# Optimization experiments

Hardware: AMD Instinct MI355X
Metric: run time of the kernel (lower is better)

## Reference

```python
import jax, jax.numpy as jnp
import numpy as np

N, C_IN, C_OUT, T, V = 64, 64, 64, 300, 25


def setup_inputs() -> dict:
    key = jax.random.key(0)
    k1, k2, k3, k4 = jax.random.split(key, 4)
    x = jax.random.normal(k1, (N, C_IN, T, V), dtype=jnp.float32)
    a = jax.random.uniform(k2, (N, T, V, V), dtype=jnp.float32)
    # 1x1 Conv2D (channels_first) == per-pixel channel-mixing matmul
    W = jax.random.normal(k3, (C_IN, C_OUT), dtype=jnp.float32) * (1.0 / np.sqrt(C_IN))
    b = jax.random.normal(k4, (C_OUT,), dtype=jnp.float32) * 0.01
    return {"x": x, "a": a, "W": W, "b": b}


def reference(x, a, W, b):
    # 1x1 conv channels_first: mix channels at every (t, v) location
    y = jnp.einsum('nctv,cd->ndtv', x, W) + b[None, :, None, None]
    # dropout in eval mode (training=False) is identity
    # spatial graph convolution: node mixing with per-(n,t) adjacency
    out = jnp.einsum('nctv,ntvw->nctw', y, a)
    return (out, a)
```

## Files before the change

kernel.cpp:

```cpp
#include <hip/hip_runtime.h>


typedef __attribute__((ext_vector_type(8))) short short8;
typedef __attribute__((ext_vector_type(4))) float f32x4;

#define XS_S 66
#define YS_S 36
#define AT_S 36

__device__ __forceinline__ unsigned short f2bf(float f) {
    unsigned int u = __builtin_bit_cast(unsigned int, f);
    return (unsigned short)((u + 0x7FFFu + ((u >> 16) & 1u)) >> 16);
}

__global__ __launch_bounds__(512, 6)
void sgcn_fused(const float* __restrict__ xg, const float* __restrict__ ag,
                const float* __restrict__ Wg, const float* __restrict__ bg,
                float* __restrict__ outg)
{
    __shared__ alignas(16) unsigned short Wt[64 * XS_S];
    __shared__ alignas(16) unsigned short At[4 * 32 * AT_S];
    __shared__ alignas(16) unsigned short Ubuf[9216];

    const int tid  = threadIdx.x;
    const int wid  = tid >> 6;
    const int lane = tid & 63;
    const int q    = lane >> 4;
    const int lo   = lane & 15;

    const int bid = blockIdx.x;
    const int n   = bid / 75;
    const int t0  = (bid % 75) * 4;

    f32x4 xv[4];
    const long xbase = ((long)n * 64 * 300 + t0) * 25;
#pragma unroll
    for (int m = 0; m < 4; ++m) {
        const int f = tid + 512 * m;
        if (m < 3 || f < 1600) {
            const int c = f / 25, j = f % 25;
            xv[m] = *(const f32x4*)(xg + xbase + (long)c * 7500 + 4 * j);
        }
    }
    f32x4 av[2];
    const long abase = ((long)n * 300 + t0) * 625;
#pragma unroll
    for (int m = 0; m < 2; ++m) {
        const int f = tid + 512 * m;
        if (m < 1 || f < 625)
            av[m] = *(const f32x4*)(ag + abase + 4 * f);
    }
    f32x4 wv[2];
#pragma unroll
    for (int m = 0; m < 2; ++m)
        wv[m] = *(const f32x4*)(Wg + 4 * (tid + 512 * m));

    if (tid < 128) {
        unsigned short* ar = &At[(tid >> 5) * (32 * AT_S) + (tid & 31) * AT_S];
#pragma unroll
        for (int i = 25; i < 32; ++i) ar[i] = 0;
    }

#pragma unroll
    for (int m = 0; m < 2; ++m) {
        const int f = 4 * (tid + 512 * m);
#pragma unroll
        for (int i = 0; i < 4; ++i) {
            const int e = f + i, c = e >> 6, d = e & 63;
            Wt[d * XS_S + c] = f2bf(wv[m][i]);
        }
    }
#pragma unroll
    for (int m = 0; m < 4; ++m) {
        const int f = tid + 512 * m;
        if (m < 3 || f < 1600) {
            const int c = f / 25, j = f % 25;
#pragma unroll
            for (int i = 0; i < 4; ++i) {
                const int e = 4 * j + i;
                const int tl = e / 25, v = e % 25;
                Ubuf[tl * (32 * XS_S) + v * XS_S + c] = f2bf(xv[m][i]);
            }
        }
    }
    {
        float* aout = outg + 30720000L + abase;
#pragma unroll
        for (int m = 0; m < 2; ++m) {
            const int f = tid + 512 * m;
            if (m < 1 || f < 625) {
                *(f32x4*)(aout + 4 * f) = av[m];
#pragma unroll
                for (int i = 0; i < 4; ++i) {
                    const int e = 4 * f + i;
                    const int tl = e / 625, r = e % 625;
                    At[tl * (32 * AT_S) + (r % 25) * AT_S + (r / 25)] = f2bf(av[m][i]);
                }
            }
        }
    }
    __syncthreads();

    const int tl = wid >> 1;
    const int dh = wid & 1;
    const int t  = t0 + tl;
    const int d0 = 32 * dh;

    short8 wfrag[2][2];
#pragma unroll
    for (int mi = 0; mi < 2; ++mi)
#pragma unroll
        for (int ki = 0; ki < 2; ++ki)
            wfrag[mi][ki] = *(const short8*)&Wt[(d0 + 16 * mi + lo) * XS_S + 32 * ki + 8 * q];

    f32x4 bias[2];
#pragma unroll
    for (int mi = 0; mi < 2; ++mi)
#pragma unroll
        for (int r = 0; r < 4; ++r)
            bias[mi][r] = bg[d0 + 16 * mi + 4 * q + r];

    const unsigned short* xs = Ubuf + tl * (32 * XS_S);
    f32x4 accy[2][2];
#pragma unroll
    for (int mi = 0; mi < 2; ++mi) { accy[mi][0] = bias[mi]; accy[mi][1] = bias[mi]; }
#pragma unroll
    for (int ni = 0; ni < 2; ++ni)
#pragma unroll
        for (int ki = 0; ki < 2; ++ki) {
            const short8 bf = *(const short8*)&xs[(16 * ni + lo) * XS_S + 32 * ki + 8 * q];
#pragma unroll
            for (int mi = 0; mi < 2; ++mi)
                accy[mi][ni] = __builtin_amdgcn_mfma_f32_16x16x32_bf16(
                    wfrag[mi][ki], bf, accy[mi][ni], 0, 0, 0);
        }

    __syncthreads();

    unsigned short* ys = Ubuf + wid * (32 * YS_S);
#pragma unroll
    for (int mi = 0; mi < 2; ++mi)
#pragma unroll
        for (int ni = 0; ni < 2; ++ni) {
            const int v = 16 * ni + lo;
            const bool ok = (v < 25);
#pragma unroll
            for (int r = 0; r < 4; ++r)
                ys[(16 * mi + 4 * q + r) * YS_S + v] =
                    ok ? f2bf(accy[mi][ni][r]) : (unsigned short)0;
        }

    const unsigned short* at = At + tl * (32 * AT_S);
    short8 afr[2];
#pragma unroll
    for (int mi = 0; mi < 2; ++mi)
        afr[mi] = *(const short8*)&at[(16 * mi + lo) * AT_S + 8 * q];
    short8 yfr[2];
#pragma unroll
    for (int dj = 0; dj < 2; ++dj)
        yfr[dj] = *(const short8*)&ys[(16 * dj + lo) * YS_S + 8 * q];

    f32x4 acco[2][2];
#pragma unroll
    for (int mi = 0; mi < 2; ++mi)
#pragma unroll
        for (int dj = 0; dj < 2; ++dj)
            acco[mi][dj] = f32x4{0.f, 0.f, 0.f, 0.f};
#pragma unroll
    for (int mi = 0; mi < 2; ++mi)
#pragma unroll
        for (int dj = 0; dj < 2; ++dj)
            acco[mi][dj] = __builtin_amdgcn_mfma_f32_16x16x32_bf16(
                afr[mi], yfr[dj], acco[mi][dj], 0, 0, 0);

    float* op = outg + ((long)n * 64 * 300 + t) * 25;
#pragma unroll
    for (int dj = 0; dj < 2; ++dj) {
        const long dbase = (long)(d0 + 16 * dj + lo) * 7500;
        *(f32x4*)(op + dbase + 4 * q) = acco[0][dj];
        if (q < 2)
            *(f32x4*)(op + dbase + 16 + 4 * q) = acco[1][dj];
        else if (q == 2)
            op[dbase + 24] = acco[1][dj][0];
    }
}

extern "C" void kernel_launch(void* const* d_in, const int* in_sizes, int n_in,
                              void* d_out, int out_size, void* d_ws, size_t ws_size,
                              hipStream_t stream) {
    const float* x = (const float*)d_in[0];
    const float* a = (const float*)d_in[1];
    const float* W = (const float*)d_in[2];
    const float* b = (const float*)d_in[3];
    float* out = (float*)d_out;
    hipLaunchKernelGGL(sgcn_fused, dim3(64 * 75), dim3(512), 0, stream,
                       x, a, W, b, out);
}
```

Measured before the change: 79.59 us.

## Process three time chunks per block with register-prefetched next chunk

Each block now handles 12 time steps in three chunks of 4 instead of one chunk, so the grid shrinks by a factor of three. Weights and bias are loaded and converted once per block, and the next chunk's x and adjacency values are prefetched into registers while the current chunk's MFMAs run. Separate LDS buffers for X and Y replace the shared union buffer, which raises LDS use, and launch bounds drop to 4 blocks per CU. The risk is lower occupancy and fewer blocks for load balance across the CUs.

```diff
diff --git a/kernel.cpp b/kernel.cpp
--- a/kernel.cpp
+++ b/kernel.cpp
@@ -13,14 +13,15 @@
     return (unsigned short)((u + 0x7FFFu + ((u >> 16) & 1u)) >> 16);
 }
 
-__global__ __launch_bounds__(512, 6)
+__global__ __launch_bounds__(512, 4)
 void sgcn_fused(const float* __restrict__ xg, const float* __restrict__ ag,
                 const float* __restrict__ Wg, const float* __restrict__ bg,
                 float* __restrict__ outg)
 {
     __shared__ alignas(16) unsigned short Wt[64 * XS_S];
+    __shared__ alignas(16) unsigned short Xs[4 * 32 * XS_S];
     __shared__ alignas(16) unsigned short At[4 * 32 * AT_S];
-    __shared__ alignas(16) unsigned short Ubuf[9216];
+    __shared__ alignas(16) unsigned short Ys[8 * 32 * YS_S];
 
     const int tid  = threadIdx.x;
     const int wid  = tid >> 6;
@@ -29,37 +30,39 @@
     const int lo   = lane & 15;
 
     const int bid = blockIdx.x;
-    const int n   = bid / 75;
-    const int t0  = (bid % 75) * 4;
-
+    const int n   = bid / 25;
+    const int t0  = (bid % 25) * 12;
+
+    f32x4 wv[2];
+#pragma unroll
+    for (int m = 0; m < 2; ++m)
+        wv[m] = *(const f32x4*)(Wg + 4 * (tid + 512 * m));
+
+    if (tid < 128) {
+        unsigned short* ar = &At[(tid >> 5) * (32 * AT_S) + (tid & 31) * AT_S];
+#pragma unroll
+        for (int i = 25; i < 32; ++i) ar[i] = 0;
+    }
+
+    long xbase = ((long)n * 64 * 300 + t0) * 25;
+    long abase = ((long)n * 300 + t0) * 625;
+
+    int xc[4], xj[4];
     f32x4 xv[4];
-    const long xbase = ((long)n * 64 * 300 + t0) * 25;
 #pragma unroll
     for (int m = 0; m < 4; ++m) {
         const int f = tid + 512 * m;
-        if (m < 3 || f < 1600) {
-            const int c = f / 25, j = f % 25;
-            xv[m] = *(const f32x4*)(xg + xbase + (long)c * 7500 + 4 * j);
-        }
+        xc[m] = f / 25; xj[m] = f % 25;
+        if (m < 3 || f < 1600)
+            xv[m] = *(const f32x4*)(xg + xbase + (long)xc[m] * 7500 + 4 * xj[m]);
     }
     f32x4 av[2];
-    const long abase = ((long)n * 300 + t0) * 625;
 #pragma unroll
     for (int m = 0; m < 2; ++m) {
         const int f = tid + 512 * m;
         if (m < 1 || f < 625)
             av[m] = *(const f32x4*)(ag + abase + 4 * f);
     }
-    f32x4 wv[2];
-#pragma unroll
-    for (int m = 0; m < 2; ++m)
-        wv[m] = *(const f32x4*)(Wg + 4 * (tid + 512 * m));
-
-    if (tid < 128) {
-        unsigned short* ar = &At[(tid >> 5) * (32 * AT_S) + (tid & 31) * AT_S];
-#pragma unroll
-        for (int i = 25; i < 32; ++i) ar[i] = 0;
-    }
 
 #pragma unroll
     for (int m = 0; m < 2; ++m) {
@@ -70,40 +73,10 @@
             Wt[d * XS_S + c] = f2bf(wv[m][i]);
         }
     }
-#pragma unroll
-    for (int m = 0; m < 4; ++m) {
-        const int f = tid + 512 * m;
-        if (m < 3 || f < 1600) {
-            const int c = f / 25, j = f % 25;
-#pragma unroll
-            for (int i = 0; i < 4; ++i) {
-                const int e = 4 * j + i;
-                const int tl = e / 25, v = e % 25;
-                Ubuf[tl * (32 * XS_S) + v * XS_S + c] = f2bf(xv[m][i]);
-            }
-        }
-    }
-    {
-        float* aout = outg + 30720000L + abase;
-#pragma unroll
-        for (int m = 0; m < 2; ++m) {
-            const int f = tid + 512 * m;
-            if (m < 1 || f < 625) {
-                *(f32x4*)(aout + 4 * f) = av[m];
-#pragma unroll
-                for (int i = 0; i < 4; ++i) {
-                    const int e = 4 * f + i;
-                    const int tl = e / 625, r = e % 625;
-                    At[tl * (32 * AT_S) + (r % 25) * AT_S + (r / 25)] = f2bf(av[m][i]);
-                }
-            }
-        }
-    }
     __syncthreads();
 
     const int tl = wid >> 1;
     const int dh = wid & 1;
-    const int t  = t0 + tl;
     const int d0 = 32 * dh;
 
     short8 wfrag[2][2];
@@ -120,68 +93,118 @@
         for (int r = 0; r < 4; ++r)
             bias[mi][r] = bg[d0 + 16 * mi + 4 * q + r];
 
-    const unsigned short* xs = Ubuf + tl * (32 * XS_S);
-    f32x4 accy[2][2];
-#pragma unroll
-    for (int mi = 0; mi < 2; ++mi) { accy[mi][0] = bias[mi]; accy[mi][1] = bias[mi]; }
-#pragma unroll
-    for (int ni = 0; ni < 2; ++ni)
-#pragma unroll
-        for (int ki = 0; ki < 2; ++ki) {
-            const short8 bf = *(const short8*)&xs[(16 * ni + lo) * XS_S + 32 * ki + 8 * q];
-#pragma unroll
-            for (int mi = 0; mi < 2; ++mi)
-                accy[mi][ni] = __builtin_amdgcn_mfma_f32_16x16x32_bf16(
-                    wfrag[mi][ki], bf, accy[mi][ni], 0, 0, 0);
-        }
-
-    __syncthreads();
-
-    unsigned short* ys = Ubuf + wid * (32 * YS_S);
-#pragma unroll
-    for (int mi = 0; mi < 2; ++mi)
-#pragma unroll
-        for (int ni = 0; ni < 2; ++ni) {
-            const int v = 16 * ni + lo;
-            const bool ok = (v < 25);
-#pragma unroll
-            for (int r = 0; r < 4; ++r)
-                ys[(16 * mi + 4 * q + r) * YS_S + v] =
-                    ok ? f2bf(accy[mi][ni][r]) : (unsigned short)0;
-        }
-
+    const unsigned short* xs = Xs + tl * (32 * XS_S);
+    unsigned short*       ys = Ys + wid * (32 * YS_S);
     const unsigned short* at = At + tl * (32 * AT_S);
-    short8 afr[2];
-#pragma unroll
-    for (int mi = 0; mi < 2; ++mi)
-        afr[mi] = *(const short8*)&at[(16 * mi + lo) * AT_S + 8 * q];
-    short8 yfr[2];
-#pragma unroll
-    for (int dj = 0; dj < 2; ++dj)
-        yfr[dj] = *(const short8*)&ys[(16 * dj + lo) * YS_S + 8 * q];
-
-    f32x4 acco[2][2];
-#pragma unroll
-    for (int mi = 0; mi < 2; ++mi)
+
+    for (int kc = 0; kc < 3; ++kc) {
+#pragma unroll
+        for (int m = 0; m < 4; ++m) {
+            const int f = tid + 512 * m;
+            if (m < 3 || f < 1600) {
+#pragma unroll
+                for (int i = 0; i < 4; ++i) {
+                    const int e = 4 * xj[m] + i;
+                    const int tc = e / 25, v = e % 25;
+                    Xs[tc * (32 * XS_S) + v * XS_S + xc[m]] = f2bf(xv[m][i]);
+                }
+            }
+        }
+        {
+            float* aout = outg + 30720000L + abase;
+#pragma unroll
+            for (int m = 0; m < 2; ++m) {
+                const int f = tid + 512 * m;
+                if (m < 1 || f < 625) {
+                    *(f32x4*)(aout + 4 * f) = av[m];
+#pragma unroll
+                    for (int i = 0; i < 4; ++i) {
+                        const int e = 4 * f + i;
+                        const int tc = e / 625, r = e % 625;
+                        At[tc * (32 * AT_S) + (r % 25) * AT_S + (r / 25)] = f2bf(av[m][i]);
+                    }
+                }
+            }
+        }
+        const int t = t0 + 4 * kc + tl;
+        __syncthreads();
+
+        if (kc < 2) {
+            xbase += 100;  abase += 2500;
+#pragma unroll
+            for (int m = 0; m < 4; ++m) {
+                const int f = tid + 512 * m;
+                if (m < 3 || f < 1600)
+                    xv[m] = *(const f32x4*)(xg + xbase + (long)xc[m] * 7500 + 4 * xj[m]);
+            }
+#pragma unroll
+            for (int m = 0; m < 2; ++m) {
+                const int f = tid + 512 * m;
+                if (m < 1 || f < 625)
+                    av[m] = *(const f32x4*)(ag + abase + 4 * f);
+            }
+        }
+
+        f32x4 accy[2][2];
+#pragma unroll
+        for (int mi = 0; mi < 2; ++mi) { accy[mi][0] = bias[mi]; accy[mi][1] = bias[mi]; }
+#pragma unroll
+        for (int ni = 0; ni < 2; ++ni)
+#pragma unroll
+            for (int ki = 0; ki < 2; ++ki) {
+                const short8 bf = *(const short8*)&xs[(16 * ni + lo) * XS_S + 32 * ki + 8 * q];
+#pragma unroll
+                for (int mi = 0; mi < 2; ++mi)
+                    accy[mi][ni] = __builtin_amdgcn_mfma_f32_16x16x32_bf16(
+                        wfrag[mi][ki], bf, accy[mi][ni], 0, 0, 0);
+            }
+
+#pragma unroll
+        for (int mi = 0; mi < 2; ++mi)
+#pragma unroll
+            for (int ni = 0; ni < 2; ++ni) {
+                const int v = 16 * ni + lo;
+                const bool ok = (v < 25);
+#pragma unroll
+                for (int r = 0; r < 4; ++r)
+                    ys[(16 * mi + 4 * q + r) * YS_S + v] =
+                        ok ? f2bf(accy[mi][ni][r]) : (unsigned short)0;
+            }
+
+        short8 afr[2];
+#pragma unroll
+        for (int mi = 0; mi < 2; ++mi)
+            afr[mi] = *(const short8*)&at[(16 * mi + lo) * AT_S + 8 * q];
+        short8 yfr[2];
 #pragma unroll
         for (int dj = 0; dj < 2; ++dj)
-            acco[mi][dj] = f32x4{0.f, 0.f, 0.f, 0.f};
-#pragma unroll
-    for (int mi = 0; mi < 2; ++mi)
-#pragma unroll
-        for (int dj = 0; dj < 2; ++dj)
-            acco[mi][dj] = __builtin_amdgcn_mfma_f32_16x16x32_bf16(
-                afr[mi], yfr[dj], acco[mi][dj], 0, 0, 0);
-
-    float* op = outg + ((long)n * 64 * 300 + t) * 25;
-#pragma unroll
-    for (int dj = 0; dj < 2; ++dj) {
-        const long dbase = (long)(d0 + 16 * dj + lo) * 7500;
-        *(f32x4*)(op + dbase + 4 * q) = acco[0][dj];
-        if (q < 2)
-            *(f32x4*)(op + dbase + 16 + 4 * q) = acco[1][dj];
-        else if (q == 2)
-            op[dbase + 24] = acco[1][dj][0];
+            yfr[dj] = *(const short8*)&ys[(16 * dj + lo) * YS_S + 8 * q];
+
+        f32x4 acco[2][2];
+#pragma unroll
+        for (int mi = 0; mi < 2; ++mi)
+#pragma unroll
+            for (int dj = 0; dj < 2; ++dj)
+                acco[mi][dj] = f32x4{0.f, 0.f, 0.f, 0.f};
+#pragma unroll
+        for (int mi = 0; mi < 2; ++mi)
+#pragma unroll
+            for (int dj = 0; dj < 2; ++dj)
+                acco[mi][dj] = __builtin_amdgcn_mfma_f32_16x16x32_bf16(
+                    afr[mi], yfr[dj], acco[mi][dj], 0, 0, 0);
+
+        float* op = outg + ((long)n * 64 * 300 + t) * 25;
+#pragma unroll
+        for (int dj = 0; dj < 2; ++dj) {
+            const long dbase = (long)(d0 + 16 * dj + lo) * 7500;
+            *(f32x4*)(op + dbase + 4 * q) = acco[0][dj];
+            if (q < 2)
+                *(f32x4*)(op + dbase + 16 + 4 * q) = acco[1][dj];
+            else if (q == 2)
+                op[dbase + 24] = acco[1][dj][0];
+        }
+
+        __syncthreads();
     }
 }
 
@@ -193,6 +216,6 @@
     const float* W = (const float*)d_in[2];
     const float* b = (const float*)d_in[3];
     float* out = (float*)d_out;
-    hipLaunchKernelGGL(sgcn_fused, dim3(64 * 75), dim3(512), 0, stream,
+    hipLaunchKernelGGL(sgcn_fused, dim3(64 * 25), dim3(512), 0, stream,
                        x, a, W, b, out);
 }
```

New measurement: 88.04 us. 1.11x slower.

## Split adjacency copy-out into dedicated blocks and separate X/Y shared buffers

Applied to the files above, without the earlier changes.

Adds 600 extra blocks, every ninth block, that only copy the adjacency tensor to its output slot, so the compute blocks no longer write it. The shared buffer that X and Y used to share becomes two separate arrays, which removes one barrier between the first GEMM and the Y stores. The cost is more shared memory per block, which may lower occupancy. The adjacency is also read twice from global memory, once by the compute blocks and once by the copy blocks.

```diff
diff --git a/kernel.cpp b/kernel.cpp
--- a/kernel.cpp
+++ b/kernel.cpp
@@ -19,19 +19,43 @@
                 float* __restrict__ outg)
 {
     __shared__ alignas(16) unsigned short Wt[64 * XS_S];
+    __shared__ alignas(16) unsigned short Xs[4 * 32 * XS_S];
+    __shared__ alignas(16) unsigned short Ys[8 * 32 * YS_S];
     __shared__ alignas(16) unsigned short At[4 * 32 * AT_S];
-    __shared__ alignas(16) unsigned short Ubuf[9216];
-
-    const int tid  = threadIdx.x;
+
+    const int tid = threadIdx.x;
+    const int bid = blockIdx.x;
+
+    if (bid % 9 == 8) {
+        const int ci = bid / 9;
+        const long base = (long)ci * 5000;
+        const float* src = ag;
+        float* dst = outg + 30720000L;
+        f32x4 v[10];
+#pragma unroll
+        for (int m = 0; m < 10; ++m) {
+            const int ib = m * 512 + tid;
+            if (ib < 5000)
+                v[m] = *(const f32x4*)(src + 4 * (base + ib));
+        }
+#pragma unroll
+        for (int m = 0; m < 10; ++m) {
+            const int ib = m * 512 + tid;
+            if (ib < 5000)
+                *(f32x4*)(dst + 4 * (base + ib)) = v[m];
+        }
+        return;
+    }
+
+    const int cb  = bid - bid / 9;
+    const int n   = cb / 75;
+    const int t0  = (cb % 75) * 4;
+
     const int wid  = tid >> 6;
     const int lane = tid & 63;
     const int q    = lane >> 4;
     const int lo   = lane & 15;
 
-    const int bid = blockIdx.x;
-    const int n   = bid / 75;
-    const int t0  = (bid % 75) * 4;
-
     f32x4 xv[4];
     const long xbase = ((long)n * 64 * 300 + t0) * 25;
 #pragma unroll
@@ -79,23 +103,19 @@
             for (int i = 0; i < 4; ++i) {
                 const int e = 4 * j + i;
                 const int tl = e / 25, v = e % 25;
-                Ubuf[tl * (32 * XS_S) + v * XS_S + c] = f2bf(xv[m][i]);
+                Xs[tl * (32 * XS_S) + v * XS_S + c] = f2bf(xv[m][i]);
             }
         }
     }
-    {
-        float* aout = outg + 30720000L + abase;
-#pragma unroll
-        for (int m = 0; m < 2; ++m) {
-            const int f = tid + 512 * m;
-            if (m < 1 || f < 625) {
-                *(f32x4*)(aout + 4 * f) = av[m];
-#pragma unroll
-                for (int i = 0; i < 4; ++i) {
-                    const int e = 4 * f + i;
-                    const int tl = e / 625, r = e % 625;
-                    At[tl * (32 * AT_S) + (r % 25) * AT_S + (r / 25)] = f2bf(av[m][i]);
-                }
+#pragma unroll
+    for (int m = 0; m < 2; ++m) {
+        const int f = tid + 512 * m;
+        if (m < 1 || f < 625) {
+#pragma unroll
+            for (int i = 0; i < 4; ++i) {
+                const int e = 4 * f + i;
+                const int tl = e / 625, r = e % 625;
+                At[tl * (32 * AT_S) + (r % 25) * AT_S + (r / 25)] = f2bf(av[m][i]);
             }
         }
     }
@@ -120,7 +140,7 @@
         for (int r = 0; r < 4; ++r)
             bias[mi][r] = bg[d0 + 16 * mi + 4 * q + r];
 
-    const unsigned short* xs = Ubuf + tl * (32 * XS_S);
+    const unsigned short* xs = Xs + tl * (32 * XS_S);
     f32x4 accy[2][2];
 #pragma unroll
     for (int mi = 0; mi < 2; ++mi) { accy[mi][0] = bias[mi]; accy[mi][1] = bias[mi]; }
@@ -135,9 +155,7 @@
                     wfrag[mi][ki], bf, accy[mi][ni], 0, 0, 0);
         }
 
-    __syncthreads();
-
-    unsigned short* ys = Ubuf + wid * (32 * YS_S);
+    unsigned short* ys = Ys + wid * (32 * YS_S);
 #pragma unroll
     for (int mi = 0; mi < 2; ++mi)
 #pragma unroll
@@ -193,6 +211,6 @@
     const float* W = (const float*)d_in[2];
     const float* b = (const float*)d_in[3];
     float* out = (float*)d_out;
-    hipLaunchKernelGGL(sgcn_fused, dim3(64 * 75), dim3(512), 0, stream,
+    hipLaunchKernelGGL(sgcn_fused, dim3(5400), dim3(512), 0, stream,
                        x, a, W, b, out);
 }
```

New measurement: 87.15 us. 9.5% more time.

## Make blocks loop over time chunks with register-prefetched, double-buffered LDS

Applied to the files above, without the earlier changes.

The kernel changes from 4800 single-chunk blocks to 512 blocks. Each block walks up to 10 chunks of 4 time steps, using double-buffered shared-memory tiles for x and the adjacency. The next chunk's global loads go into registers while the current chunk's MFMAs run, which is meant to hide load latency and to amortize the W transpose, bias loads and index math across chunks. The cost is fewer blocks (two per CU at most, with an uneven last slice of 5 chunks) and higher register and LDS use per block, so latency hiding may suffer.

```diff
diff --git a/kernel.cpp b/kernel.cpp
--- a/kernel.cpp
+++ b/kernel.cpp
@@ -7,20 +7,23 @@
 #define XS_S 66
 #define YS_S 36
 #define AT_S 36
+#define XBUF (4 * 32 * XS_S)
+#define ABUF (4 * 32 * AT_S)
 
 __device__ __forceinline__ unsigned short f2bf(float f) {
     unsigned int u = __builtin_bit_cast(unsigned int, f);
     return (unsigned short)((u + 0x7FFFu + ((u >> 16) & 1u)) >> 16);
 }
 
-__global__ __launch_bounds__(512, 6)
-void sgcn_fused(const float* __restrict__ xg, const float* __restrict__ ag,
-                const float* __restrict__ Wg, const float* __restrict__ bg,
-                float* __restrict__ outg)
+__global__ __launch_bounds__(512, 4)
+void sgcn_persist(const float* __restrict__ xg, const float* __restrict__ ag,
+                  const float* __restrict__ Wg, const float* __restrict__ bg,
+                  float* __restrict__ outg)
 {
     __shared__ alignas(16) unsigned short Wt[64 * XS_S];
-    __shared__ alignas(16) unsigned short At[4 * 32 * AT_S];
-    __shared__ alignas(16) unsigned short Ubuf[9216];
+    __shared__ alignas(16) unsigned short Xs[2][XBUF];
+    __shared__ alignas(16) unsigned short At[2][ABUF];
+    __shared__ alignas(16) unsigned short Ys[8 * 32 * YS_S];
 
     const int tid  = threadIdx.x;
     const int wid  = tid >> 6;
@@ -29,81 +32,72 @@
     const int lo   = lane & 15;
 
     const int bid = blockIdx.x;
-    const int n   = bid / 75;
-    const int t0  = (bid % 75) * 4;
-
-    f32x4 xv[4];
-    const long xbase = ((long)n * 64 * 300 + t0) * 25;
+    const int n   = bid >> 3;
+    const int s   = bid & 7;
+    const int t0  = 40 * s;
+    const int nch = (s < 7) ? 10 : 5;
+
+    int xgoff[4], offx[4][4];
+    bool vxm[4];
 #pragma unroll
     for (int m = 0; m < 4; ++m) {
         const int f = tid + 512 * m;
-        if (m < 3 || f < 1600) {
-            const int c = f / 25, j = f % 25;
-            xv[m] = *(const f32x4*)(xg + xbase + (long)c * 7500 + 4 * j);
-        }
-    }
-    f32x4 av[2];
-    const long abase = ((long)n * 300 + t0) * 625;
+        vxm[m] = (m < 3) || (tid < 64);
+        const int c = f / 25, j = f % 25;
+        xgoff[m] = c * 7500 + 4 * j;
+#pragma unroll
+        for (int i = 0; i < 4; ++i) {
+            const int e = 4 * j + i;
+            offx[m][i] = (e / 25) * (32 * XS_S) + (e % 25) * XS_S + c;
+        }
+    }
+    int agoff[2], offa[2][4];
+    bool vam[2];
 #pragma unroll
     for (int m = 0; m < 2; ++m) {
-        const int f = tid + 512 * m;
-        if (m < 1 || f < 625)
-            av[m] = *(const f32x4*)(ag + abase + 4 * f);
-    }
+        const int af = tid + 512 * m;
+        vam[m] = (m < 1) || (tid < 113);
+        agoff[m] = 4 * af;
+#pragma unroll
+        for (int i = 0; i < 4; ++i) {
+            const int e = 4 * af + i;
+            const int tc = e / 625, r = e % 625;
+            offa[m][i] = tc * (32 * AT_S) + (r % 25) * AT_S + (r / 25);
+        }
+    }
+
+    const float* xb = xg + n * 480000 + t0 * 25;
+    const float* ab = ag + n * 187500 + t0 * 625;
+    float*       ao = outg + 30720000 + n * 187500 + t0 * 625;
+
+    f32x4 xv[4], av[2];
+#pragma unroll
+    for (int m = 0; m < 4; ++m) if (vxm[m]) xv[m] = *(const f32x4*)(xb + xgoff[m]);
+#pragma unroll
+    for (int m = 0; m < 2; ++m) if (vam[m]) av[m] = *(const f32x4*)(ab + agoff[m]);
+
     f32x4 wv[2];
 #pragma unroll
-    for (int m = 0; m < 2; ++m)
-        wv[m] = *(const f32x4*)(Wg + 4 * (tid + 512 * m));
-
-    if (tid < 128) {
-        unsigned short* ar = &At[(tid >> 5) * (32 * AT_S) + (tid & 31) * AT_S];
+    for (int m = 0; m < 2; ++m) wv[m] = *(const f32x4*)(Wg + 4 * (tid + 512 * m));
+
+    if (tid < 256) {
+        unsigned short* ar = &At[tid >> 7][(tid & 127) * AT_S];
 #pragma unroll
         for (int i = 25; i < 32; ++i) ar[i] = 0;
     }
-
 #pragma unroll
     for (int m = 0; m < 2; ++m) {
-        const int f = 4 * (tid + 512 * m);
+        const int e0 = 4 * (tid + 512 * m);
 #pragma unroll
         for (int i = 0; i < 4; ++i) {
-            const int e = f + i, c = e >> 6, d = e & 63;
-            Wt[d * XS_S + c] = f2bf(wv[m][i]);
-        }
-    }
-#pragma unroll
-    for (int m = 0; m < 4; ++m) {
-        const int f = tid + 512 * m;
-        if (m < 3 || f < 1600) {
-            const int c = f / 25, j = f % 25;
-#pragma unroll
-            for (int i = 0; i < 4; ++i) {
-                const int e = 4 * j + i;
-                const int tl = e / 25, v = e % 25;
-                Ubuf[tl * (32 * XS_S) + v * XS_S + c] = f2bf(xv[m][i]);
-            }
-        }
-    }
-    {
-        float* aout = outg + 30720000L + abase;
-#pragma unroll
-        for (int m = 0; m < 2; ++m) {
-            const int f = tid + 512 * m;
-            if (m < 1 || f < 625) {
-                *(f32x4*)(aout + 4 * f) = av[m];
-#pragma unroll
-                for (int i = 0; i < 4; ++i) {
-                    const int e = 4 * f + i;
-                    const int tl = e / 625, r = e % 625;
-                    At[tl * (32 * AT_S) + (r % 25) * AT_S + (r / 25)] = f2bf(av[m][i]);
-                }
-            }
+            const int e = e0 + i;
+            Wt[(e & 63) * XS_S + (e >> 6)] = f2bf(wv[m][i]);
         }
     }
     __syncthreads();
 
     const int tl = wid >> 1;
     const int dh = wid & 1;
-    const int t  = t0 + tl;
     const int d0 = 32 * dh;
 
     short8 wfrag[2][2];
@@ -120,68 +114,95 @@
         for (int r = 0; r < 4; ++r)
             bias[mi][r] = bg[d0 + 16 * mi + 4 * q + r];
 
-    const unsigned short* xs = Ubuf + tl * (32 * XS_S);
-    f32x4 accy[2][2];
-#pragma unroll
-    for (int mi = 0; mi < 2; ++mi) { accy[mi][0] = bias[mi]; accy[mi][1] = bias[mi]; }
-#pragma unroll
-    for (int ni = 0; ni < 2; ++ni)
-#pragma unroll
-        for (int ki = 0; ki < 2; ++ki) {
-            const short8 bf = *(const short8*)&xs[(16 * ni + lo) * XS_S + 32 * ki + 8 * q];
-#pragma unroll
-            for (int mi = 0; mi < 2; ++mi)
-                accy[mi][ni] = __builtin_amdgcn_mfma_f32_16x16x32_bf16(
-                    wfrag[mi][ki], bf, accy[mi][ni], 0, 0, 0);
-        }
-
-    __syncthreads();
-
-    unsigned short* ys = Ubuf + wid * (32 * YS_S);
-#pragma unroll
-    for (int mi = 0; mi < 2; ++mi)
-#pragma unroll
-        for (int ni = 0; ni < 2; ++ni) {
-            const int v = 16 * ni + lo;
-            const bool ok = (v < 25);
-#pragma unroll
-            for (int r = 0; r < 4; ++r)
-                ys[(16 * mi + 4 * q + r) * YS_S + v] =
-                    ok ? f2bf(accy[mi][ni][r]) : (unsigned short)0;
-        }
-
-    const unsigned short* at = At + tl * (32 * AT_S);
-    short8 afr[2];
-#pragma unroll
-    for (int mi = 0; mi < 2; ++mi)
-        afr[mi] = *(const short8*)&at[(16 * mi + lo) * AT_S + 8 * q];
-    short8 yfr[2];
-#pragma unroll
-    for (int dj = 0; dj < 2; ++dj)
-        yfr[dj] = *(const short8*)&ys[(16 * dj + lo) * YS_S + 8 * q];
-
-    f32x4 acco[2][2];
-#pragma unroll
-    for (int mi = 0; mi < 2; ++mi)
+    unsigned short* ys = Ys + wid * (32 * YS_S);
+    const int outb = n * 480000;
+
+    for (int kc = 0; kc < nch; ++kc) {
+        unsigned short* xbuf = Xs[kc & 1];
+        unsigned short* abuf = At[kc & 1];
+
+#pragma unroll
+        for (int m = 0; m < 4; ++m) if (vxm[m]) {
+#pragma unroll
+            for (int i = 0; i < 4; ++i) xbuf[offx[m][i]] = f2bf(xv[m][i]);
+        }
+#pragma unroll
+        for (int m = 0; m < 2; ++m) if (vam[m]) {
+            *(f32x4*)(ao + agoff[m]) = av[m];
+#pragma unroll
+            for (int i = 0; i < 4; ++i) abuf[offa[m][i]] = f2bf(av[m][i]);
+        }
+        __syncthreads();
+
+        if (kc + 1 < nch) {
+            xb += 100; ab += 2500; ao += 2500;
+#pragma unroll
+            for (int m = 0; m < 4; ++m) if (vxm[m]) xv[m] = *(const f32x4*)(xb + xgoff[m]);
+#pragma unroll
+            for (int m = 0; m < 2; ++m) if (vam[m]) av[m] = *(const f32x4*)(ab + agoff[m]);
+        }
+
+        const unsigned short* xs = xbuf + tl * (32 * XS_S);
+        f32x4 accy[2][2];
+#pragma unroll
+        for (int mi = 0; mi < 2; ++mi) { accy[mi][0] = bias[mi]; accy[mi][1] = bias[mi]; }
+#pragma unroll
+        for (int ni = 0; ni < 2; ++ni)
+#pragma unroll
+            for (int ki = 0; ki < 2; ++ki) {
+                const short8 bf = *(const short8*)&xs[(16 * ni + lo) * XS_S + 32 * ki + 8 * q];
+#pragma unroll
+                for (int mi = 0; mi < 2; ++mi)
+                    accy[mi][ni] = __builtin_amdgcn_mfma_f32_16x16x32_bf16(
+                        wfrag[mi][ki], bf, accy[mi][ni], 0, 0, 0);
+            }
+
+#pragma unroll
+        for (int mi = 0; mi < 2; ++mi)
+#pragma unroll
+            for (int ni = 0; ni < 2; ++ni) {
+                const int v = 16 * ni + lo;
+                const bool ok = (v < 25);
+#pragma unroll
+                for (int r = 0; r < 4; ++r)
+                    ys[(16 * mi + 4 * q + r) * YS_S + v] =
+                        ok ? f2bf(accy[mi][ni][r]) : (unsigned short)0;
+            }
+
+        const unsigned short* at = abuf + tl * (32 * AT_S);
+        short8 afr[2];
+#pragma unroll
+        for (int mi = 0; mi < 2; ++mi)
+            afr[mi] = *(const short8*)&at[(16 * mi + lo) * AT_S + 8 * q];
+        short8 yfr[2];
 #pragma unroll
         for (int dj = 0; dj < 2; ++dj)
-            acco[mi][dj] = f32x4{0.f, 0.f, 0.f, 0.f};
-#pragma unroll
-    for (int mi = 0; mi < 2; ++mi)
-#pragma unroll
-        for (int dj = 0; dj < 2; ++dj)
-            acco[mi][dj] = __builtin_amdgcn_mfma_f32_16x16x32_bf16(
-                afr[mi], yfr[dj], acco[mi][dj], 0, 0, 0);
-
-    float* op = outg + ((long)n * 64 * 300 + t) * 25;
-#pragma unroll
-    for (int dj = 0; dj < 2; ++dj) {
-        const long dbase = (long)(d0 + 16 * dj + lo) * 7500;
-        *(f32x4*)(op + dbase + 4 * q) = acco[0][dj];
-        if (q < 2)
-            *(f32x4*)(op + dbase + 16 + 4 * q) = acco[1][dj];
-        else if (q == 2)
-            op[dbase + 24] = acco[1][dj][0];
+            yfr[dj] = *(const short8*)&ys[(16 * dj + lo) * YS_S + 8 * q];
+
+        f32x4 acco[2][2];
+#pragma unroll
+        for (int mi = 0; mi < 2; ++mi)
+#pragma unroll
+            for (int dj = 0; dj < 2; ++dj)
+                acco[mi][dj] = f32x4{0.f, 0.f, 0.f, 0.f};
+#pragma unroll
+        for (int mi = 0; mi < 2; ++mi)
+#pragma unroll
+            for (int dj = 0; dj < 2; ++dj)
+                acco[mi][dj] = __builtin_amdgcn_mfma_f32_16x16x32_bf16(
+                    afr[mi], yfr[dj], acco[mi][dj], 0, 0, 0);
+
+        const int t = t0 + 4 * kc + tl;
+        float* op = outg + outb + t * 25;
+#pragma unroll
+        for (int dj = 0; dj < 2; ++dj) {
+            const int dbase = (d0 + 16 * dj + lo) * 7500;
+            *(f32x4*)(op + dbase + 4 * q) = acco[0][dj];
+            if (q < 2)
+                *(f32x4*)(op + dbase + 16 + 4 * q) = acco[1][dj];
+            else if (q == 2)
+                op[dbase + 24] = acco[1][dj][0];
+        }
     }
 }
 
@@ -193,6 +214,6 @@
     const float* W = (const float*)d_in[2];
     const float* b = (const float*)d_in[3];
     float* out = (float*)d_out;
-    hipLaunchKernelGGL(sgcn_fused, dim3(64 * 75), dim3(512), 0, stream,
+    hipLaunchKernelGGL(sgcn_persist, dim3(512), dim3(512), 0, stream,
                        x, a, W, b, out);
 }
```

After: 127.1 us. +59.7%, slower.
